# Optimization experiments

Measured on AMD Instinct MI355X. Metric: run time of the kernel, lower is better.

The kernel has to match this reference:

```python
import jax, jax.numpy as jnp
import numpy as np
import math

DIM_Q = 512; DIM_K = 512; DIM_V = 512; H = 8; EPS = 1e-5

def _layernorm(x, g, b):
    mu = jnp.mean(x, axis=-1, keepdims=True)
    var = jnp.mean((x - mu) ** 2, axis=-1, keepdims=True)
    return (x - mu) * jax.lax.rsqrt(var + EPS) * g + b

def setup_inputs() -> dict:
    key = jax.random.key(0)
    ks = jax.random.split(key, 12)
    B, NQ, NK = 8, 1024, 1024
    s = 0.02
    return {
        "Q": jax.random.normal(ks[0], (B, NQ, DIM_Q), jnp.float32),
        "K": jax.random.normal(ks[1], (B, NK, DIM_K), jnp.float32),
        "attention_mask": jax.random.randint(ks[2], (B, NK), 0, 2, jnp.int32),
        "Wq": jax.random.normal(ks[3], (DIM_Q, DIM_V), jnp.float32) * s,
        "bq": jnp.zeros((DIM_V,), jnp.float32),
        "Wk": jax.random.normal(ks[4], (DIM_K, DIM_V), jnp.float32) * s,
        "bk": jnp.zeros((DIM_V,), jnp.float32),
        "Wv": jax.random.normal(ks[5], (DIM_K, DIM_V), jnp.float32) * s,
        "bv": jnp.zeros((DIM_V,), jnp.float32),
        "Wo": jax.random.normal(ks[6], (DIM_V, DIM_V), jnp.float32) * s,
        "bo": jnp.zeros((DIM_V,), jnp.float32),
        "g0": jnp.ones((DIM_V,), jnp.float32),
        "b0": jnp.zeros((DIM_V,), jnp.float32),
        "g1": jnp.ones((DIM_V,), jnp.float32),
        "b1": jnp.zeros((DIM_V,), jnp.float32),
    }

def reference(Q, K, attention_mask, Wq, bq, Wk, bk, Wv, bv, Wo, bo, g0, b0, g1, b1):
    B, NQ, _ = Q.shape
    NK = K.shape[1]
    dh = DIM_V // H
    q = (Q @ Wq + bq).reshape(B, NQ, H, dh).transpose(0, 2, 1, 3)  # (B,H,NQ,dh)
    k = (K @ Wk + bk).reshape(B, NK, H, dh).transpose(0, 2, 1, 3)
    v = (K @ Wv + bv).reshape(B, NK, H, dh).transpose(0, 2, 1, 3)
    # NOTE: original scales by sqrt(dim_V), not sqrt(head_dim)
    scores = jnp.einsum("bhqd,bhkd->bhqk", q, k) / math.sqrt(DIM_V)
    scores = jnp.where(attention_mask[:, None, None, :] == 0, -10000.0, scores)
    A = jax.nn.softmax(scores, axis=-1)
    o = q + jnp.einsum("bhqk,bhkd->bhqd", A, v)  # residual before output proj
    O = o.transpose(0, 2, 1, 3).reshape(B, NQ, DIM_V)
    O = _layernorm(O, g0, b0)
    O = O + jax.nn.relu(O @ Wo + bo)
    O = _layernorm(O, g1, b1)
    return O
```

## Files before the change

### kernel.cpp

```cpp
#include <hip/hip_runtime.h>

typedef __attribute__((ext_vector_type(8))) short short8;
typedef __attribute__((ext_vector_type(4))) short short4v;
typedef __attribute__((ext_vector_type(4))) float float4v;

#define LDT 72
#define SCALE 0.044194173824159216f

__device__ inline unsigned short f2b(float f) {
    unsigned u = __float_as_uint(f);
    return (unsigned short)((u + 0x7FFFu + ((u >> 16) & 1u)) >> 16);
}
__device__ inline float b2f(unsigned short s) {
    return __uint_as_float(((unsigned)s) << 16);
}

__global__ void cast_bf16_kernel(const float* __restrict__ in,
                                 unsigned short* __restrict__ out, int n) {
    int i = (blockIdx.x * blockDim.x + threadIdx.x) * 8;
    if (i < n) {
        float4v a = *(const float4v*)(in + i);
        float4v b = *(const float4v*)(in + i + 4);
        short8 o;
        o[0] = (short)f2b(a[0]); o[1] = (short)f2b(a[1]);
        o[2] = (short)f2b(a[2]); o[3] = (short)f2b(a[3]);
        o[4] = (short)f2b(b[0]); o[5] = (short)f2b(b[1]);
        o[6] = (short)f2b(b[2]); o[7] = (short)f2b(b[3]);
        *(short8*)(out + i) = o;
    }
}

__global__ void transpose_w_kernel(const float* __restrict__ W0, const float* __restrict__ W1,
                                   const float* __restrict__ W2, const float* __restrict__ W3,
                                   unsigned short* __restrict__ out) {
    const float* W = (blockIdx.z == 0) ? W0 : (blockIdx.z == 1) ? W1
                   : (blockIdx.z == 2) ? W2 : W3;
    unsigned short* o = out + (size_t)blockIdx.z * 512 * 512;
    __shared__ float tile[32][33];
    int k0 = blockIdx.x * 32, n0 = blockIdx.y * 32;
    int tx = threadIdx.x & 31, ty = threadIdx.x >> 5;
    for (int r = ty; r < 32; r += 8) tile[r][tx] = W[(size_t)(k0 + r) * 512 + n0 + tx];
    __syncthreads();
    for (int r = ty; r < 32; r += 8) o[(size_t)(n0 + r) * 512 + k0 + tx] = f2b(tile[tx][r]);
}

__global__ __launch_bounds__(256) void gemm_kernel(
    const unsigned short* __restrict__ Qb, const unsigned short* __restrict__ Kb,
    const unsigned short* __restrict__ hb, const unsigned short* __restrict__ WT,
    const float* __restrict__ bq, const float* __restrict__ bk,
    const float* __restrict__ bv, const float* __restrict__ bo,
    unsigned short* __restrict__ qo, unsigned short* __restrict__ ko,
    unsigned short* __restrict__ vTo, unsigned short* __restrict__ to_,
    int zbase) {
    int z = zbase + blockIdx.z;
    const unsigned short* A = (z == 0) ? Qb : (z == 3) ? hb : Kb;
    const unsigned short* BT = WT + (size_t)z * 512 * 512;
    const float* bias = (z == 0) ? bq : (z == 1) ? bk : (z == 2) ? bv : bo;

    __shared__ unsigned short As[128 * LDT];
    __shared__ unsigned short Bs[128 * LDT];

    int tid = threadIdx.x;
    int lane = tid & 63, wave = tid >> 6;
    int wr = wave >> 1, wc = wave & 1;
    int l15 = lane & 15, lg = lane >> 4;
    int row0 = blockIdx.x * 128, col0 = blockIdx.y * 128;

    float4v acc[4][4];
#pragma unroll
    for (int m = 0; m < 4; m++)
#pragma unroll
        for (int n = 0; n < 4; n++) acc[m][n] = (float4v){0.f, 0.f, 0.f, 0.f};

    int sr = tid >> 3, sc = (tid & 7) * 8;

    for (int k0 = 0; k0 < 512; k0 += 64) {
        __syncthreads();
#pragma unroll
        for (int i = 0; i < 4; i++) {
            int r = sr + 32 * i;
            *(short8*)(As + r * LDT + sc) =
                *(const short8*)(A + (size_t)(row0 + r) * 512 + k0 + sc);
            *(short8*)(Bs + r * LDT + sc) =
                *(const short8*)(BT + (size_t)(col0 + r) * 512 + k0 + sc);
        }
        __syncthreads();
#pragma unroll
        for (int kk = 0; kk < 2; kk++) {
            short8 af[4], bf[4];
#pragma unroll
            for (int m = 0; m < 4; m++)
                af[m] = *(const short8*)(As + (wr * 64 + m * 16 + l15) * LDT + kk * 32 + lg * 8);
#pragma unroll
            for (int n = 0; n < 4; n++)
                bf[n] = *(const short8*)(Bs + (wc * 64 + n * 16 + l15) * LDT + kk * 32 + lg * 8);
#pragma unroll
            for (int m = 0; m < 4; m++)
#pragma unroll
                for (int n = 0; n < 4; n++)
                    acc[m][n] = __builtin_amdgcn_mfma_f32_16x16x32_bf16(af[m], bf[n], acc[m][n], 0, 0, 0);
        }
    }

#pragma unroll
    for (int n = 0; n < 4; n++) {
        int col = col0 + wc * 64 + n * 16 + l15;
        float bias_v = bias[col];
#pragma unroll
        for (int m = 0; m < 4; m++) {
            int rowb = row0 + wr * 64 + m * 16 + lg * 4;
            float4v v = acc[m][n];
            if (z == 2) {
                int b = rowb >> 10, tq = rowb & 1023;
                int h = col >> 6, d = col & 63;
                short4v st;
#pragma unroll
                for (int r = 0; r < 4; r++) st[r] = (short)f2b(v[r] + bias_v);
                *(short4v*)(vTo + ((((size_t)b * 8 + h) * 64 + d) << 10) + tq) = st;
            } else if (z == 3) {
#pragma unroll
                for (int r = 0; r < 4; r++) {
                    size_t idx = (size_t)(rowb + r) * 512 + col;
                    float x = v[r] + bias_v;
                    x = x > 0.f ? x : 0.f;
                    to_[idx] = f2b(x + b2f(hb[idx]));
                }
            } else {
                unsigned short* o = (z == 0) ? qo : ko;
#pragma unroll
                for (int r = 0; r < 4; r++)
                    o[(size_t)(rowb + r) * 512 + col] = f2b(v[r] + bias_v);
            }
        }
    }
}

__global__ __launch_bounds__(256) void attn_kernel(
    const unsigned short* __restrict__ qb, const unsigned short* __restrict__ kb,
    const unsigned short* __restrict__ vT, const int* __restrict__ mask,
    unsigned short* __restrict__ ob) {
    __shared__ unsigned short Ks[64 * LDT];
    __shared__ unsigned short Vs[64 * LDT];
    __shared__ unsigned short Ps[64 * LDT];
    __shared__ int ms[64];

    int tid = threadIdx.x;
    int lane = tid & 63, wave = tid >> 6;
    int l15 = lane & 15, lg = lane >> 4;
    int bh = blockIdx.y;
    int b = bh >> 3, h = bh & 7;
    int qrow0 = b * 1024 + blockIdx.x * 64 + wave * 16;

    short8 qf[2];
#pragma unroll
    for (int kk = 0; kk < 2; kk++)
        qf[kk] = *(const short8*)(qb + (size_t)(qrow0 + l15) * 512 + h * 64 + kk * 32 + lg * 8);

    float m_run[4], l_run[4];
    float4v oacc[4];
#pragma unroll
    for (int r = 0; r < 4; r++) { m_run[r] = -1e30f; l_run[r] = 0.f; }
#pragma unroll
    for (int n = 0; n < 4; n++) oacc[n] = (float4v){0.f, 0.f, 0.f, 0.f};

    int stok = tid >> 2, scoff = (tid & 3) * 16;
    unsigned short* pw = Ps + wave * 16 * LDT;

    for (int jt = 0; jt < 16; jt++) {
        __syncthreads();
        {
            const unsigned short* kg =
                kb + (size_t)(b * 1024 + jt * 64 + stok) * 512 + h * 64 + scoff;
            *(short8*)(Ks + stok * LDT + scoff) = *(const short8*)kg;
            *(short8*)(Ks + stok * LDT + scoff + 8) = *(const short8*)(kg + 8);
            const unsigned short* vg =
                vT + (((size_t)bh * 64 + stok) << 10) + jt * 64 + scoff;
            *(short8*)(Vs + stok * LDT + scoff) = *(const short8*)vg;
            *(short8*)(Vs + stok * LDT + scoff + 8) = *(const short8*)(vg + 8);
            if (tid < 64) ms[tid] = mask[b * 1024 + jt * 64 + tid];
        }
        __syncthreads();

        float4v s[4];
#pragma unroll
        for (int jf = 0; jf < 4; jf++) {
            short8 kf0 = *(const short8*)(Ks + (jf * 16 + l15) * LDT + lg * 8);
            short8 kf1 = *(const short8*)(Ks + (jf * 16 + l15) * LDT + 32 + lg * 8);
            float4v t = (float4v){0.f, 0.f, 0.f, 0.f};
            t = __builtin_amdgcn_mfma_f32_16x16x32_bf16(qf[0], kf0, t, 0, 0, 0);
            t = __builtin_amdgcn_mfma_f32_16x16x32_bf16(qf[1], kf1, t, 0, 0, 0);
            s[jf] = t;
        }
#pragma unroll
        for (int jf = 0; jf < 4; jf++) {
            float mb = ms[jf * 16 + l15] ? 0.f : -10000.f;
#pragma unroll
            for (int r = 0; r < 4; r++) s[jf][r] = s[jf][r] * SCALE + mb;
        }
#pragma unroll
        for (int r = 0; r < 4; r++) {
            float mx = fmaxf(fmaxf(s[0][r], s[1][r]), fmaxf(s[2][r], s[3][r]));
#pragma unroll
            for (int off = 1; off < 16; off <<= 1) mx = fmaxf(mx, __shfl_xor(mx, off));
            float mnew = fmaxf(m_run[r], mx);
            float sf = __expf(m_run[r] - mnew);
            m_run[r] = mnew;
            float ps = 0.f;
#pragma unroll
            for (int jf = 0; jf < 4; jf++) {
                float p = __expf(s[jf][r] - mnew);
                s[jf][r] = p;
                ps += p;
            }
#pragma unroll
            for (int off = 1; off < 16; off <<= 1) ps += __shfl_xor(ps, off);
            l_run[r] = l_run[r] * sf + ps;
#pragma unroll
            for (int n = 0; n < 4; n++) oacc[n][r] *= sf;
        }
#pragma unroll
        for (int jf = 0; jf < 4; jf++)
#pragma unroll
            for (int r = 0; r < 4; r++)
                pw[(lg * 4 + r) * LDT + jf * 16 + l15] = f2b(s[jf][r]);

        short8 pa0 = *(const short8*)(pw + l15 * LDT + lg * 8);
        short8 pa1 = *(const short8*)(pw + l15 * LDT + 32 + lg * 8);
#pragma unroll
        for (int n = 0; n < 4; n++) {
            short8 vf0 = *(const short8*)(Vs + (n * 16 + l15) * LDT + lg * 8);
            short8 vf1 = *(const short8*)(Vs + (n * 16 + l15) * LDT + 32 + lg * 8);
            oacc[n] = __builtin_amdgcn_mfma_f32_16x16x32_bf16(pa0, vf0, oacc[n], 0, 0, 0);
            oacc[n] = __builtin_amdgcn_mfma_f32_16x16x32_bf16(pa1, vf1, oacc[n], 0, 0, 0);
        }
    }

#pragma unroll
    for (int n = 0; n < 4; n++) {
        int gcol = h * 64 + n * 16 + l15;
#pragma unroll
        for (int r = 0; r < 4; r++) {
            size_t idx = (size_t)(qrow0 + lg * 4 + r) * 512 + gcol;
            float val = oacc[n][r] / l_run[r];
            ob[idx] = f2b(b2f(qb[idx]) + val);
        }
    }
}

__global__ void ln_kernel_bf16(const unsigned short* __restrict__ in,
                               const float* __restrict__ g, const float* __restrict__ bb,
                               unsigned short* __restrict__ out) {
    int row = blockIdx.x, lane = threadIdx.x;
    short8 v = *(const short8*)(in + (size_t)row * 512 + lane * 8);
    float x[8], s = 0.f, s2 = 0.f;
#pragma unroll
    for (int j = 0; j < 8; j++) {
        x[j] = b2f((unsigned short)v[j]);
        s += x[j];
        s2 += x[j] * x[j];
    }
#pragma unroll
    for (int off = 1; off < 64; off <<= 1) {
        s += __shfl_xor(s, off);
        s2 += __shfl_xor(s2, off);
    }
    float mu = s * (1.f / 512.f);
    float var = s2 * (1.f / 512.f) - mu * mu;
    float rs = rsqrtf(var + 1e-5f);
#pragma unroll
    for (int j = 0; j < 8; j++) {
        int c = lane * 8 + j;
        out[(size_t)row * 512 + c] = f2b((x[j] - mu) * rs * g[c] + bb[c]);
    }
}

__global__ void ln_kernel_f32(const unsigned short* __restrict__ in,
                              const float* __restrict__ g, const float* __restrict__ bb,
                              float* __restrict__ out) {
    int row = blockIdx.x, lane = threadIdx.x;
    short8 v = *(const short8*)(in + (size_t)row * 512 + lane * 8);
    float x[8], s = 0.f, s2 = 0.f;
#pragma unroll
    for (int j = 0; j < 8; j++) {
        x[j] = b2f((unsigned short)v[j]);
        s += x[j];
        s2 += x[j] * x[j];
    }
#pragma unroll
    for (int off = 1; off < 64; off <<= 1) {
        s += __shfl_xor(s, off);
        s2 += __shfl_xor(s2, off);
    }
    float mu = s * (1.f / 512.f);
    float var = s2 * (1.f / 512.f) - mu * mu;
    float rs = rsqrtf(var + 1e-5f);
#pragma unroll
    for (int j = 0; j < 8; j++) {
        int c = lane * 8 + j;
        out[(size_t)row * 512 + c] = (x[j] - mu) * rs * g[c] + bb[c];
    }
}

extern "C" void kernel_launch(void* const* d_in, const int* in_sizes, int n_in,
                              void* d_out, int out_size, void* d_ws, size_t ws_size,
                              hipStream_t stream) {
    const float* Q = (const float*)d_in[0];
    const float* K = (const float*)d_in[1];
    const int* mask = (const int*)d_in[2];
    const float* Wq = (const float*)d_in[3];
    const float* bq = (const float*)d_in[4];
    const float* Wk = (const float*)d_in[5];
    const float* bk = (const float*)d_in[6];
    const float* Wv = (const float*)d_in[7];
    const float* bv = (const float*)d_in[8];
    const float* Wo = (const float*)d_in[9];
    const float* bo = (const float*)d_in[10];
    const float* g0 = (const float*)d_in[11];
    const float* b0 = (const float*)d_in[12];
    const float* g1 = (const float*)d_in[13];
    const float* b1 = (const float*)d_in[14];
    float* out = (float*)d_out;

    const size_t N = 8192ull * 512;
    unsigned short* w16 = (unsigned short*)d_ws;
    unsigned short* Qb = w16;
    unsigned short* Kb = Qb + N;
    unsigned short* WT = Kb + N;
    unsigned short* qb = WT + 4ull * 512 * 512;
    unsigned short* kb = qb + N;
    unsigned short* vTb = kb + N;
    unsigned short* obuf = vTb + N;
    unsigned short* hbuf = obuf + N;
    unsigned short* tbuf = hbuf + N;

    cast_bf16_kernel<<<2048, 256, 0, stream>>>(Q, Qb, (int)N);
    cast_bf16_kernel<<<2048, 256, 0, stream>>>(K, Kb, (int)N);
    transpose_w_kernel<<<dim3(16, 16, 4), 256, 0, stream>>>(Wq, Wk, Wv, Wo, WT);
    gemm_kernel<<<dim3(64, 4, 3), 256, 0, stream>>>(Qb, Kb, hbuf, WT, bq, bk, bv, bo,
                                                    qb, kb, vTb, tbuf, 0);
    attn_kernel<<<dim3(16, 64), 256, 0, stream>>>(qb, kb, vTb, mask, obuf);
    ln_kernel_bf16<<<8192, 64, 0, stream>>>(obuf, g0, b0, hbuf);
    gemm_kernel<<<dim3(64, 4, 1), 256, 0, stream>>>(Qb, Kb, hbuf, WT, bq, bk, bv, bo,
                                                    qb, kb, vTb, tbuf, 3);
    ln_kernel_f32<<<8192, 64, 0, stream>>>(tbuf, g1, b1, out);
}
```

Before: 226.9 us.

## Compute transposed attention tiles in registers to drop P shared-memory round trip

The attention kernel swaps MFMA operand order so each lane holds one query row's scores across the key dimension. K rows are permuted in shared memory so the probability fragment can feed the PV MFMA directly from registers, which removes the Ps LDS buffer and its write/read. Softmax reductions shrink to two cross-lane shuffles with scalar running max and sum per lane. The mask is precomputed to a float bias, f2b uses the hip bf16 intrinsic with packed stores, and the output epilogue writes vectorised short4 stores. The cost is a more intricate index permutation that must match the MFMA layout exactly.

```diff
diff --git a/kernel.cpp b/kernel.cpp
--- a/kernel.cpp
+++ b/kernel.cpp
@@ -1,18 +1,22 @@
 #include <hip/hip_runtime.h>
+#include <hip/hip_bf16.h>
 
 typedef __attribute__((ext_vector_type(8))) short short8;
 typedef __attribute__((ext_vector_type(4))) short short4v;
 typedef __attribute__((ext_vector_type(4))) float float4v;
+typedef __attribute__((ext_vector_type(4))) unsigned uint4v;
 
 #define LDT 72
 #define SCALE 0.044194173824159216f
 
 __device__ inline unsigned short f2b(float f) {
-    unsigned u = __float_as_uint(f);
-    return (unsigned short)((u + 0x7FFFu + ((u >> 16) & 1u)) >> 16);
+    return __builtin_bit_cast(unsigned short, __float2bfloat16(f));
 }
 __device__ inline float b2f(unsigned short s) {
     return __uint_as_float(((unsigned)s) << 16);
+}
+__device__ inline unsigned pk2(float lo, float hi) {
+    return (unsigned)f2b(lo) | ((unsigned)f2b(hi) << 16);
 }
 
 __global__ void cast_bf16_kernel(const float* __restrict__ in,
@@ -21,12 +25,8 @@
     if (i < n) {
         float4v a = *(const float4v*)(in + i);
         float4v b = *(const float4v*)(in + i + 4);
-        short8 o;
-        o[0] = (short)f2b(a[0]); o[1] = (short)f2b(a[1]);
-        o[2] = (short)f2b(a[2]); o[3] = (short)f2b(a[3]);
-        o[4] = (short)f2b(b[0]); o[5] = (short)f2b(b[1]);
-        o[6] = (short)f2b(b[2]); o[7] = (short)f2b(b[3]);
-        *(short8*)(out + i) = o;
+        uint4v o = {pk2(a[0], a[1]), pk2(a[2], a[3]), pk2(b[0], b[1]), pk2(b[2], b[3])};
+        *(uint4v*)(out + i) = o;
     }
 }
 
@@ -141,8 +141,7 @@
     unsigned short* __restrict__ ob) {
     __shared__ unsigned short Ks[64 * LDT];
     __shared__ unsigned short Vs[64 * LDT];
-    __shared__ unsigned short Ps[64 * LDT];
-    __shared__ int ms[64];
+    __shared__ float mbias[64];
 
     int tid = threadIdx.x;
     int lane = tid & 63, wave = tid >> 6;
@@ -156,94 +155,98 @@
     for (int kk = 0; kk < 2; kk++)
         qf[kk] = *(const short8*)(qb + (size_t)(qrow0 + l15) * 512 + h * 64 + kk * 32 + lg * 8);
 
-    float m_run[4], l_run[4];
+    float m_run = -1e30f, l_run = 0.f;
     float4v oacc[4];
 #pragma unroll
-    for (int r = 0; r < 4; r++) { m_run[r] = -1e30f; l_run[r] = 0.f; }
-#pragma unroll
     for (int n = 0; n < 4; n++) oacc[n] = (float4v){0.f, 0.f, 0.f, 0.f};
 
     int stok = tid >> 2, scoff = (tid & 3) * 16;
-    unsigned short* pw = Ps + wave * 16 * LDT;
+    int prow = (stok & 0x23) | ((stok & 4) << 2) | ((stok & 0x18) >> 1);
 
     for (int jt = 0; jt < 16; jt++) {
         __syncthreads();
         {
             const unsigned short* kg =
                 kb + (size_t)(b * 1024 + jt * 64 + stok) * 512 + h * 64 + scoff;
-            *(short8*)(Ks + stok * LDT + scoff) = *(const short8*)kg;
-            *(short8*)(Ks + stok * LDT + scoff + 8) = *(const short8*)(kg + 8);
+            *(short8*)(Ks + prow * LDT + scoff) = *(const short8*)kg;
+            *(short8*)(Ks + prow * LDT + scoff + 8) = *(const short8*)(kg + 8);
             const unsigned short* vg =
                 vT + (((size_t)bh * 64 + stok) << 10) + jt * 64 + scoff;
             *(short8*)(Vs + stok * LDT + scoff) = *(const short8*)vg;
             *(short8*)(Vs + stok * LDT + scoff + 8) = *(const short8*)(vg + 8);
-            if (tid < 64) ms[tid] = mask[b * 1024 + jt * 64 + tid];
+            if (tid < 64) mbias[tid] = mask[b * 1024 + jt * 64 + tid] ? 0.f : -10000.f;
         }
         __syncthreads();
 
-        float4v s[4];
+        float p[4][4];
 #pragma unroll
         for (int jf = 0; jf < 4; jf++) {
             short8 kf0 = *(const short8*)(Ks + (jf * 16 + l15) * LDT + lg * 8);
             short8 kf1 = *(const short8*)(Ks + (jf * 16 + l15) * LDT + 32 + lg * 8);
             float4v t = (float4v){0.f, 0.f, 0.f, 0.f};
-            t = __builtin_amdgcn_mfma_f32_16x16x32_bf16(qf[0], kf0, t, 0, 0, 0);
-            t = __builtin_amdgcn_mfma_f32_16x16x32_bf16(qf[1], kf1, t, 0, 0, 0);
-            s[jf] = t;
-        }
-#pragma unroll
-        for (int jf = 0; jf < 4; jf++) {
-            float mb = ms[jf * 16 + l15] ? 0.f : -10000.f;
-#pragma unroll
-            for (int r = 0; r < 4; r++) s[jf][r] = s[jf][r] * SCALE + mb;
-        }
-#pragma unroll
-        for (int r = 0; r < 4; r++) {
-            float mx = fmaxf(fmaxf(s[0][r], s[1][r]), fmaxf(s[2][r], s[3][r]));
-#pragma unroll
-            for (int off = 1; off < 16; off <<= 1) mx = fmaxf(mx, __shfl_xor(mx, off));
-            float mnew = fmaxf(m_run[r], mx);
-            float sf = __expf(m_run[r] - mnew);
-            m_run[r] = mnew;
-            float ps = 0.f;
-#pragma unroll
-            for (int jf = 0; jf < 4; jf++) {
-                float p = __expf(s[jf][r] - mnew);
-                s[jf][r] = p;
-                ps += p;
+            t = __builtin_amdgcn_mfma_f32_16x16x32_bf16(kf0, qf[0], t, 0, 0, 0);
+            t = __builtin_amdgcn_mfma_f32_16x16x32_bf16(kf1, qf[1], t, 0, 0, 0);
+#pragma unroll
+            for (int r = 0; r < 4; r++) p[jf][r] = t[r];
+        }
+        float mx = -1e30f;
+#pragma unroll
+        for (int jf = 0; jf < 4; jf++)
+#pragma unroll
+            for (int r = 0; r < 4; r++) {
+                float val = fmaf(p[jf][r], SCALE,
+                                 mbias[32 * (jf >> 1) + 8 * lg + 4 * (jf & 1) + r]);
+                p[jf][r] = val;
+                mx = fmaxf(mx, val);
             }
-#pragma unroll
-            for (int off = 1; off < 16; off <<= 1) ps += __shfl_xor(ps, off);
-            l_run[r] = l_run[r] * sf + ps;
-#pragma unroll
-            for (int n = 0; n < 4; n++) oacc[n][r] *= sf;
-        }
+        mx = fmaxf(mx, __shfl_xor(mx, 16));
+        mx = fmaxf(mx, __shfl_xor(mx, 32));
+        float mnew = fmaxf(m_run, mx);
+        float sf = __expf(m_run - mnew);
+        m_run = mnew;
+        float ps = 0.f;
 #pragma unroll
         for (int jf = 0; jf < 4; jf++)
 #pragma unroll
-            for (int r = 0; r < 4; r++)
-                pw[(lg * 4 + r) * LDT + jf * 16 + l15] = f2b(s[jf][r]);
-
-        short8 pa0 = *(const short8*)(pw + l15 * LDT + lg * 8);
-        short8 pa1 = *(const short8*)(pw + l15 * LDT + 32 + lg * 8);
+            for (int r = 0; r < 4; r++) {
+                float e = __expf(p[jf][r] - mnew);
+                p[jf][r] = e;
+                ps += e;
+            }
+        ps += __shfl_xor(ps, 16);
+        ps += __shfl_xor(ps, 32);
+        l_run = l_run * sf + ps;
+#pragma unroll
+        for (int n = 0; n < 4; n++)
+#pragma unroll
+            for (int r = 0; r < 4; r++) oacc[n][r] *= sf;
+
+        uint4v w0 = {pk2(p[0][0], p[0][1]), pk2(p[0][2], p[0][3]),
+                     pk2(p[1][0], p[1][1]), pk2(p[1][2], p[1][3])};
+        uint4v w1 = {pk2(p[2][0], p[2][1]), pk2(p[2][2], p[2][3]),
+                     pk2(p[3][0], p[3][1]), pk2(p[3][2], p[3][3])};
+        short8 pb0 = __builtin_bit_cast(short8, w0);
+        short8 pb1 = __builtin_bit_cast(short8, w1);
+
 #pragma unroll
         for (int n = 0; n < 4; n++) {
             short8 vf0 = *(const short8*)(Vs + (n * 16 + l15) * LDT + lg * 8);
             short8 vf1 = *(const short8*)(Vs + (n * 16 + l15) * LDT + 32 + lg * 8);
-            oacc[n] = __builtin_amdgcn_mfma_f32_16x16x32_bf16(pa0, vf0, oacc[n], 0, 0, 0);
-            oacc[n] = __builtin_amdgcn_mfma_f32_16x16x32_bf16(pa1, vf1, oacc[n], 0, 0, 0);
-        }
-    }
-
+            oacc[n] = __builtin_amdgcn_mfma_f32_16x16x32_bf16(vf0, pb0, oacc[n], 0, 0, 0);
+            oacc[n] = __builtin_amdgcn_mfma_f32_16x16x32_bf16(vf1, pb1, oacc[n], 0, 0, 0);
+        }
+    }
+
+    float inv = 1.f / l_run;
 #pragma unroll
     for (int n = 0; n < 4; n++) {
-        int gcol = h * 64 + n * 16 + l15;
-#pragma unroll
-        for (int r = 0; r < 4; r++) {
-            size_t idx = (size_t)(qrow0 + lg * 4 + r) * 512 + gcol;
-            float val = oacc[n][r] / l_run[r];
-            ob[idx] = f2b(b2f(qb[idx]) + val);
-        }
+        size_t base = (size_t)(qrow0 + l15) * 512 + h * 64 + n * 16 + lg * 4;
+        short4v qr = *(const short4v*)(qb + base);
+        short4v st;
+#pragma unroll
+        for (int r = 0; r < 4; r++)
+            st[r] = (short)f2b(b2f((unsigned short)qr[r]) + oacc[n][r] * inv);
+        *(short4v*)(ob + base) = st;
     }
 }
 
```

After: 211.1 us. -6.9%, faster.
